# Optimization experiments

Measured on AMD Instinct MI355X. Metric: run time of the kernel, lower is better.

Reference implementation:

```python
import jax, jax.numpy as jnp
import numpy as np

B, T, D, H = 1, 4096, 1024, 16
DK = D // H
SCALE = 1.0 / float(np.sqrt(DK))
NEG = -1e9


def setup_inputs() -> dict:
    key = jax.random.key(0)
    k1, k2, k3 = jax.random.split(key, 3)
    x = jax.random.normal(k1, (B, T, D), dtype=jnp.float32)
    # xavier-ish small weights (gain 0.5)
    Wqkv = jax.random.normal(k2, (3 * D, D), dtype=jnp.float32) * 0.02
    Wout = jax.random.normal(k3, (D, D), dtype=jnp.float32) * 0.02
    return {"x": x, "Wqkv": Wqkv, "Wout": Wout}


def reference(x, Wqkv, Wout):
    b, t, d = x.shape
    # QKV projection (no bias): [B,T,3D] -> [3,B,H,T,DK]
    qkv = jnp.einsum('btd,ed->bte', x, Wqkv)
    qkv = qkv.reshape(b, t, 3, H, DK).transpose(2, 0, 3, 1, 4)
    q, k, v = qkv[0], qkv[1], qkv[2]
    # scaled dot-product scores, clamped
    scores = jnp.einsum('bhtd,bhsd->bhts', q, k) * SCALE
    scores = jnp.clip(scores, -10.0, 10.0)
    # causal additive mask (strict upper triangle gets -1e9)
    mask = jnp.triu(jnp.full((t, t), NEG, dtype=scores.dtype), k=1)
    scores = scores + mask[None, None, :, :]
    attn = jax.nn.softmax(scores, axis=-1)  # dropout is identity in eval
    out = jnp.einsum('bhts,bhsd->bhtd', attn, v)
    out = out.transpose(0, 2, 1, 3).reshape(b, t, d)
    return jnp.einsum('btd,ed->bte', out, Wout)
```

## Files before the change

kernel.cpp:

```cpp
#include <hip/hip_runtime.h>

#define T_SEQ   4096
#define D_MODEL 1024
#define NH      16
#define HD      64
#define E3      3072
#define QSCL    0.125f
#define TILEB   (64L*E3)
#define SLOTSZ  8448

using u32x2  = __attribute__((ext_vector_type(2))) unsigned int;
using u32x4  = __attribute__((ext_vector_type(4))) unsigned int;
using u16x4  = __attribute__((ext_vector_type(4))) unsigned short;
using u16x8  = __attribute__((ext_vector_type(8))) unsigned short;
using u64x2  = __attribute__((ext_vector_type(2))) unsigned long long;
using f32x4  = __attribute__((ext_vector_type(4))) float;
using bf16x8 = __attribute__((ext_vector_type(8))) __bf16;

__device__ __forceinline__ unsigned short f2bf(float f){
  unsigned int u = __builtin_bit_cast(unsigned int, f);
  u += 0x7fffu + ((u >> 16) & 1u);
  return (unsigned short)(u >> 16);
}
__device__ __forceinline__ float bf2f(unsigned short v){
  unsigned int u = ((unsigned int)v) << 16;
  return __builtin_bit_cast(float, u);
}

__device__ __forceinline__ void gload_lds16(const void* g, void* l){
  __builtin_amdgcn_global_load_lds((const __attribute__((address_space(1))) void*)g,
                                   (__attribute__((address_space(3))) void*)l, 16, 0, 0);
}

#define XN4   (T_SEQ*D_MODEL/4)
#define WQN4  (E3*D_MODEL/4)
#define WON4  (D_MODEL*D_MODEL/4)
__global__ __launch_bounds__(256) void cvt_all(const float4* __restrict__ x,
                                               const float4* __restrict__ wq,
                                               const float4* __restrict__ wo,
                                               u16x4* __restrict__ xb,
                                               u16x4* __restrict__ wqb,
                                               u16x4* __restrict__ wob){
  int i = blockIdx.x * 256 + threadIdx.x;
  const float4* src; u16x4* dst; int j;
  if(i < XN4){ src = x;  dst = xb;  j = i; }
  else if(i < XN4 + WQN4){ src = wq; dst = wqb; j = i - XN4; }
  else { src = wo; dst = wob; j = i - XN4 - WQN4; }
  float4 v = src[j];
  u16x4 o = { f2bf(v.x), f2bf(v.y), f2bf(v.z), f2bf(v.w) };
  dst[j] = o;
}

template<int OUT_BF16, int QSCALE>
__global__ __launch_bounds__(256) void gemm_bt(const unsigned short* __restrict__ A,
                                               const unsigned short* __restrict__ B,
                                               void* __restrict__ Cv,
                                               int M, int N, int K){
  __shared__ unsigned short As[128*32];
  __shared__ unsigned short Bs[128*32];
  const int t    = threadIdx.x;
  const int lane = t & 63;
  const int w    = t >> 6;
  const int brow = blockIdx.y * 128;
  const int bcol = blockIdx.x * 128;
  const int wrow = (w >> 1) * 64;
  const int wcol = (w & 1) * 64;
  const int cc = lane & 15;
  const int gg = lane >> 4;

  f32x4 acc[4][4];
  #pragma unroll
  for(int m=0;m<4;++m)
    #pragma unroll
    for(int n=0;n<4;++n)
      acc[m][n] = (f32x4){0.f,0.f,0.f,0.f};

  const int srow = t >> 2;
  const int sk   = (t & 3) * 8;
  const long aBase = (long)(brow + srow) * K;
  const long bBase = (long)(bcol + srow) * K;

  for(int k0 = 0; k0 < K; k0 += 32){
    __syncthreads();
    gload_lds16(A + aBase + k0 + sk,               As + t*8);
    gload_lds16(A + aBase + 64*(long)K + k0 + sk,  As + 2048 + t*8);
    gload_lds16(B + bBase + k0 + sk,               Bs + t*8);
    gload_lds16(B + bBase + 64*(long)K + k0 + sk,  Bs + 2048 + t*8);
    __syncthreads();

    bf16x8 af[4], bfr[4];
    #pragma unroll
    for(int m=0;m<4;++m)
      af[m]  = *(const bf16x8*)((const char*)As + (wrow + m*16 + cc)*64 + gg*16);
    #pragma unroll
    for(int n=0;n<4;++n)
      bfr[n] = *(const bf16x8*)((const char*)Bs + (wcol + n*16 + cc)*64 + gg*16);
    #pragma unroll
    for(int m=0;m<4;++m)
      #pragma unroll
      for(int n=0;n<4;++n)
        acc[m][n] = __builtin_amdgcn_mfma_f32_16x16x32_bf16(af[m], bfr[n], acc[m][n], 0, 0, 0);
  }

  #pragma unroll
  for(int m=0;m<4;++m){
    #pragma unroll
    for(int n=0;n<4;++n){
      const int row0 = brow + wrow + m*16 + gg*4;
      const int col  = bcol + wcol + n*16 + cc;
      const float sc = (QSCALE && col < D_MODEL) ? QSCL : 1.0f;
      #pragma unroll
      for(int r=0;r<4;++r){
        if constexpr (OUT_BF16 != 0){
          ((unsigned short*)Cv)[(long)(row0 + r)*N + col] = f2bf(acc[m][n][r] * sc);
        } else {
          ((float*)Cv)[(long)(row0 + r)*N + col] = acc[m][n][r];
        }
      }
    }
  }
}

__global__ __launch_bounds__(256) void gemm_bt64(const unsigned short* __restrict__ A,
                                                 const unsigned short* __restrict__ B,
                                                 float* __restrict__ C,
                                                 int M, int N, int K){
  __shared__ unsigned short As[64*32];
  __shared__ unsigned short Bs[128*32];
  const int t    = threadIdx.x;
  const int lane = t & 63;
  const int w    = t >> 6;
  const int brow = blockIdx.y * 64;
  const int bcol = blockIdx.x * 128;
  const int wrow = (w >> 1) * 32;
  const int wcol = (w & 1) * 64;
  const int cc = lane & 15;
  const int gg = lane >> 4;

  f32x4 acc[2][4];
  #pragma unroll
  for(int m=0;m<2;++m)
    #pragma unroll
    for(int n=0;n<4;++n)
      acc[m][n] = (f32x4){0.f,0.f,0.f,0.f};

  const int srow = t >> 2;
  const int sk   = (t & 3) * 8;
  const long aBase = (long)(brow + srow) * K;
  const long bBase = (long)(bcol + srow) * K;

  for(int k0 = 0; k0 < K; k0 += 32){
    __syncthreads();
    gload_lds16(A + aBase + k0 + sk,               As + t*8);
    gload_lds16(B + bBase + k0 + sk,               Bs + t*8);
    gload_lds16(B + bBase + 64*(long)K + k0 + sk,  Bs + 2048 + t*8);
    __syncthreads();

    bf16x8 af[2], bfr[4];
    #pragma unroll
    for(int m=0;m<2;++m)
      af[m]  = *(const bf16x8*)((const char*)As + (wrow + m*16 + cc)*64 + gg*16);
    #pragma unroll
    for(int n=0;n<4;++n)
      bfr[n] = *(const bf16x8*)((const char*)Bs + (wcol + n*16 + cc)*64 + gg*16);
    #pragma unroll
    for(int m=0;m<2;++m)
      #pragma unroll
      for(int n=0;n<4;++n)
        acc[m][n] = __builtin_amdgcn_mfma_f32_16x16x32_bf16(af[m], bfr[n], acc[m][n], 0, 0, 0);
  }

  #pragma unroll
  for(int m=0;m<2;++m){
    #pragma unroll
    for(int n=0;n<4;++n){
      const int row0 = brow + wrow + m*16 + gg*4;
      const int col  = bcol + wcol + n*16 + cc;
      #pragma unroll
      for(int r=0;r<4;++r)
        C[(long)(row0 + r)*N + col] = acc[m][n][r];
    }
  }
}

__global__ __launch_bounds__(256, 5) void attn_part(const unsigned short* __restrict__ qkv,
                                                    unsigned short* __restrict__ attnb,
                                                    char* __restrict__ parts){
  __shared__ char LB[32768];

  const int t    = threadIdx.x;
  const int lane = t & 63;
  const int w    = t >> 6;
  const int cc   = lane & 15;
  const int gg   = lane >> 4;

  const int bid  = blockIdx.x;
  const int hd   = bid & 15;
  const int item = 175 - (bid >> 4);

  int qb, t0, n, slot;
  if(item < 16){
    qb = item; t0 = 0; n = qb + 1; slot = -1;
  } else if(item < 48){
    const int i = item - 16; qb = 16 + (i >> 1); const int hf = i & 1;
    const int n0 = qb + 1, h0 = (n0 + 1) >> 1;
    t0 = hf ? h0 : 0; n = hf ? (n0 - h0) : h0;
    slot = (hd*16 + (qb-16))*2 + hf;
  } else {
    const int i = item - 48; qb = 32 + (i >> 2); const int qt = i & 3;
    const int n0 = qb + 1, bsz = n0 >> 2, rem = n0 & 3;
    t0 = qt*bsz + (qt < rem ? qt : rem);
    n  = bsz + (qt < rem ? 1 : 0);
    slot = 512 + (hd*32 + (qb-32))*4 + qt;
  }
  const int q0w = qb*64 + w*16;

  bf16x8 bq0 = *(const bf16x8*)(qkv + (long)(q0w+cc)*E3 + hd*HD +      gg*8);
  bf16x8 bq1 = *(const bf16x8*)(qkv + (long)(q0w+cc)*E3 + hd*HD + 32 + gg*8);

  const f32x4 z4 = (f32x4){0.f,0.f,0.f,0.f};
  const bf16x8 ones = __builtin_bit_cast(bf16x8,
      (u32x4){0x3F803F80u,0x3F803F80u,0x3F803F80u,0x3F803F80u});

  f32x4 acc0 = z4, acc1 = z4, acc2 = z4, acc3 = z4, rsacc = z4;

  const bool lb0 = (4*gg + 0) > cc;
  const bool lb1 = (4*gg + 1) > cc;
  const bool lb2 = (4*gg + 2) > cc;
  const bool lb3 = (4*gg + 3) > cc;

  const int kOffA = cc*128 + (((gg    ) ^ (cc&7)) << 4);
  const int kOffB = cc*128 + (((gg + 4) ^ (cc&7)) << 4);

  const unsigned ldsBase = (unsigned)(unsigned long long)(&LB[0]);
  const unsigned vA0 = ldsBase + 8192  + lane*8;
  const unsigned vA1 = ldsBase + 24576 + lane*8;

  const int kLane0 = (t>>3)*E3 + D_MODEL + hd*HD + (((t&7) ^ ((t>>3)&7)) << 3);
  const int kLane1 = kLane0 + 32*E3;
  const int vLane0 = (4*((t>>3)&15) + ((t&7)>>1))*E3 + 2*D_MODEL + hd*HD
                     + ((2*(t>>7) + (t&1)) << 3);
  const int vLane1 = vLane0 + 32;

  #define STAGE(g_, BUF) do{                                                       \
    const unsigned short* gb_ = qkv + (long)(g_)*TILEB;                            \
    gload_lds16(gb_ + kLane0, LB + (BUF)*16384 + t*16);                            \
    gload_lds16(gb_ + kLane1, LB + (BUF)*16384 + 4096  + t*16);                    \
    gload_lds16(gb_ + vLane0, LB + (BUF)*16384 + 8192  + t*16);                    \
    gload_lds16(gb_ + vLane1, LB + (BUF)*16384 + 12288 + t*16);                    \
  }while(0)

  #define TRRD(d_, va_, OFF_)                                                      \
    asm volatile("ds_read_b64_tr_b16 %0, %1 offset:%c2"                            \
                 : "=v"(d_) : "v"(va_), "i"(OFF_))

  #define PVH(pa_, vab_, H)                                                        \
  {                                                                                \
    unsigned long long q0_,q1_,q2_,q3_,q4_,q5_,q6_,q7_;                            \
    TRRD(q0_, vab_, (H)*1024 + 0);    TRRD(q1_, vab_, (H)*1024 + 512);             \
    TRRD(q2_, vab_, (H)*1024 + 2048); TRRD(q3_, vab_, (H)*1024 + 2560);            \
    TRRD(q4_, vab_, (H)*1024 + 4096); TRRD(q5_, vab_, (H)*1024 + 4608);            \
    TRRD(q6_, vab_, (H)*1024 + 6144); TRRD(q7_, vab_, (H)*1024 + 6656);            \
    asm volatile("s_waitcnt lgkmcnt(0)");                                          \
    __builtin_amdgcn_sched_barrier(0);                                             \
    rsacc = __builtin_amdgcn_mfma_f32_16x16x32_bf16(pa_, ones, rsacc, 0,0,0);      \
    u64x2 p0_ = {q0_,q1_};                                                         \
    acc0 = __builtin_amdgcn_mfma_f32_16x16x32_bf16(pa_, __builtin_bit_cast(bf16x8,p0_), acc0, 0,0,0); \
    u64x2 p1_ = {q2_,q3_};                                                         \
    acc1 = __builtin_amdgcn_mfma_f32_16x16x32_bf16(pa_, __builtin_bit_cast(bf16x8,p1_), acc1, 0,0,0); \
    u64x2 p2_ = {q4_,q5_};                                                         \
    acc2 = __builtin_amdgcn_mfma_f32_16x16x32_bf16(pa_, __builtin_bit_cast(bf16x8,p2_), acc2, 0,0,0); \
    u64x2 p3_ = {q6_,q7_};                                                         \
    acc3 = __builtin_amdgcn_mfma_f32_16x16x32_bf16(pa_, __builtin_bit_cast(bf16x8,p3_), acc3, 0,0,0); \
  }

  #define TILE(g_, BUF)                                                            \
  {                                                                                \
    STAGE((g_)+1, (BUF)^1);                                                        \
    float pk[4][4];                                                                \
    const bool last_ = ((g_) == qb);                                               \
    if(!last_){                                                                    \
      _Pragma("unroll")                                                            \
      for(int kt=0; kt<4; ++kt){                                                   \
        bf16x8 a0 = *(const bf16x8*)(LB + (BUF)*16384 + kOffA + kt*2048);          \
        bf16x8 a1 = *(const bf16x8*)(LB + (BUF)*16384 + kOffB + kt*2048);          \
        f32x4 s = __builtin_amdgcn_mfma_f32_16x16x32_bf16(a0, bq0, z4, 0,0,0);     \
        s = __builtin_amdgcn_mfma_f32_16x16x32_bf16(a1, bq1, s, 0,0,0);            \
        pk[kt][0] = __expf(__builtin_amdgcn_fmed3f(s[0],-10.f,10.f));              \
        pk[kt][1] = __expf(__builtin_amdgcn_fmed3f(s[1],-10.f,10.f));              \
        pk[kt][2] = __expf(__builtin_amdgcn_fmed3f(s[2],-10.f,10.f));              \
        pk[kt][3] = __expf(__builtin_amdgcn_fmed3f(s[3],-10.f,10.f));              \
      }                                                                            \
    } else {                                                                       \
      _Pragma("unroll")                                                            \
      for(int kt=0; kt<4; ++kt){                                                   \
        if(kt <= w){                                                               \
          bf16x8 a0 = *(const bf16x8*)(LB + (BUF)*16384 + kOffA + kt*2048);        \
          bf16x8 a1 = *(const bf16x8*)(LB + (BUF)*16384 + kOffB + kt*2048);        \
          f32x4 s = __builtin_amdgcn_mfma_f32_16x16x32_bf16(a0, bq0, z4, 0,0,0);   \
          s = __builtin_amdgcn_mfma_f32_16x16x32_bf16(a1, bq1, s, 0,0,0);          \
          float p0_ = __expf(__builtin_amdgcn_fmed3f(s[0],-10.f,10.f));            \
          float p1_ = __expf(__builtin_amdgcn_fmed3f(s[1],-10.f,10.f));            \
          float p2_ = __expf(__builtin_amdgcn_fmed3f(s[2],-10.f,10.f));            \
          float p3_ = __expf(__builtin_amdgcn_fmed3f(s[3],-10.f,10.f));            \
          if(kt == w){                                                             \
            p0_ = lb0 ? 0.f : p0_;  p1_ = lb1 ? 0.f : p1_;                         \
            p2_ = lb2 ? 0.f : p2_;  p3_ = lb3 ? 0.f : p3_;                         \
          }                                                                        \
          pk[kt][0]=p0_; pk[kt][1]=p1_; pk[kt][2]=p2_; pk[kt][3]=p3_;              \
        } else {                                                                   \
          pk[kt][0]=0.f; pk[kt][1]=0.f; pk[kt][2]=0.f; pk[kt][3]=0.f;              \
        }                                                                          \
      }                                                                            \
    }                                                                              \
    bf16x8 pa0 = (bf16x8){ (__bf16)pk[0][0],(__bf16)pk[0][1],(__bf16)pk[0][2],     \
      (__bf16)pk[0][3],(__bf16)pk[1][0],(__bf16)pk[1][1],(__bf16)pk[1][2],         \
      (__bf16)pk[1][3] };                                                          \
    bf16x8 pa1 = (bf16x8){ (__bf16)pk[2][0],(__bf16)pk[2][1],(__bf16)pk[2][2],     \
      (__bf16)pk[2][3],(__bf16)pk[3][0],(__bf16)pk[3][1],(__bf16)pk[3][2],         \
      (__bf16)pk[3][3] };                                                          \
    const unsigned vab_ = (BUF) ? vA1 : vA0;                                       \
    PVH(pa0, vab_, 0);                                                             \
    if(!last_ || w >= 2){ PVH(pa1, vab_, 1); }                                     \
    __syncthreads();                                                               \
  }

  STAGE(t0, 0);
  __syncthreads();

  int lt = 0;
  while(lt + 2 <= n){
    TILE(t0+lt,   0);
    TILE(t0+lt+1, 1);
    lt += 2;
  }
  if(lt < n) TILE(t0+lt, 0);

  if(slot < 0){
    #pragma unroll
    for(int rr=0;rr<4;++rr){
      const float inv = 1.0f / rsacc[rr];
      const int row = q0w + 4*gg + rr;
      unsigned short* dst = attnb + (long)row*D_MODEL + hd*HD + cc;
      dst[0]  = __builtin_bit_cast(unsigned short, (__bf16)(acc0[rr]*inv));
      dst[16] = __builtin_bit_cast(unsigned short, (__bf16)(acc1[rr]*inv));
      dst[32] = __builtin_bit_cast(unsigned short, (__bf16)(acc2[rr]*inv));
      dst[48] = __builtin_bit_cast(unsigned short, (__bf16)(acc3[rr]*inv));
    }
  } else {
    char* sp = parts + (size_t)slot * SLOTSZ;
    #pragma unroll
    for(int rr=0;rr<4;++rr){
      const int row = w*16 + 4*gg + rr;
      unsigned short* dst = (unsigned short*)sp + row*64 + cc;
      dst[0]  = f2bf(acc0[rr]);
      dst[16] = f2bf(acc1[rr]);
      dst[32] = f2bf(acc2[rr]);
      dst[48] = f2bf(acc3[rr]);
      if(cc == 0) ((float*)(sp + 8192))[row] = rsacc[rr];
    }
  }
  #undef STAGE
  #undef TRRD
  #undef PVH
  #undef TILE
}

__global__ __launch_bounds__(256) void attn_combine(const char* __restrict__ parts,
                                                    unsigned short* __restrict__ attnb){
  const int b  = blockIdx.x;
  const int hd = b & 15;
  const int qb = 16 + (b >> 4);
  const int t  = threadIdx.x;
  const int r  = t >> 2;
  const int d0 = (t & 3) * 16;

  const char* p0; int np;
  if(qb < 32){ p0 = parts + (size_t)((hd*16 + (qb-16))*2) * SLOTSZ;        np = 2; }
  else       { p0 = parts + (size_t)(512 + (hd*32 + (qb-32))*4) * SLOTSZ;  np = 4; }

  float rs = 0.f;
  float o[16];
  #pragma unroll
  for(int j=0;j<16;++j) o[j] = 0.f;

  for(int pi = 0; pi < np; ++pi){
    const char* pp = p0 + (size_t)pi * SLOTSZ;
    rs += ((const float*)(pp + 8192))[r];
    u16x8 a0 = *(const u16x8*)(pp + (r*64 + d0)*2);
    u16x8 a1 = *(const u16x8*)(pp + (r*64 + d0)*2 + 16);
    #pragma unroll
    for(int j=0;j<8;++j){ o[j] += bf2f(a0[j]); o[8+j] += bf2f(a1[j]); }
  }
  const float inv = 1.0f / rs;
  u16x8 o0, o1;
  #pragma unroll
  for(int j=0;j<8;++j){ o0[j] = f2bf(o[j]*inv); o1[j] = f2bf(o[8+j]*inv); }
  unsigned short* dst = attnb + (long)(qb*64 + r)*D_MODEL + hd*HD + d0;
  *(u16x8*)(dst)     = o0;
  *(u16x8*)(dst + 8) = o1;
}

extern "C" void kernel_launch(void* const* d_in, const int* in_sizes, int n_in,
                              void* d_out, int out_size, void* d_ws, size_t ws_size,
                              hipStream_t stream){
  (void)in_sizes; (void)n_in; (void)out_size; (void)ws_size;
  const float* x    = (const float*)d_in[0];
  const float* wqkv = (const float*)d_in[1];
  const float* wout = (const float*)d_in[2];
  char* ws = (char*)d_ws;
  unsigned short* woutb = (unsigned short*)(ws);
  unsigned short* attnb = (unsigned short*)(ws + (2u  << 20));
  unsigned short* qkvb  = (unsigned short*)(ws + (10u << 20));
  unsigned short* xb    = (unsigned short*)(ws + (34u << 20));
  unsigned short* wqkvb = (unsigned short*)(ws + (42u << 20));
  char*           parts = ws + (34u << 20);
  float* out = (float*)d_out;

  cvt_all<<<dim3((XN4 + WQN4 + WON4)/256), 256, 0, stream>>>(
      (const float4*)x, (const float4*)wqkv, (const float4*)wout,
      (u16x4*)xb, (u16x4*)wqkvb, (u16x4*)woutb);

  dim3 g1(E3/128, T_SEQ/128);
  gemm_bt<1,1><<<g1, 256, 0, stream>>>(xb, wqkvb, qkvb, T_SEQ, E3, D_MODEL);

  attn_part<<<dim3(176*NH), 256, 0, stream>>>(qkvb, attnb, parts);
  attn_combine<<<dim3(48*NH), 256, 0, stream>>>(parts, attnb);

  dim3 g3(D_MODEL/128, T_SEQ/64);
  gemm_bt64<<<g3, 256, 0, stream>>>(attnb, woutb, out, T_SEQ, D_MODEL, D_MODEL);
}
```

Measured before the change: 127.9 us.

## Software-pipeline attention loop: overlap next tile QK/softmax with current PV

Restructures the attention inner loop so the QK^T scores and softmax for tile i+1 are computed while the PV MFMAs for tile i are issued, interleaving LDS reads and matrix ops. K and V staging are split into separate double-buffered LDS regions, with K prefetched two tiles ahead and V one tile ahead. The aim is to hide exp/softmax latency and LDS read latency behind MFMA work. It costs extra registers for the carried probability fragments and uses more complex buffer indexing, which may lower occupancy.

```diff
diff --git a/kernel.cpp b/kernel.cpp
--- a/kernel.cpp
+++ b/kernel.cpp
@@ -224,16 +224,11 @@
 
   f32x4 acc0 = z4, acc1 = z4, acc2 = z4, acc3 = z4, rsacc = z4;
 
-  const bool lb0 = (4*gg + 0) > cc;
-  const bool lb1 = (4*gg + 1) > cc;
-  const bool lb2 = (4*gg + 2) > cc;
-  const bool lb3 = (4*gg + 3) > cc;
-
   const int kOffA = cc*128 + (((gg    ) ^ (cc&7)) << 4);
   const int kOffB = cc*128 + (((gg + 4) ^ (cc&7)) << 4);
 
   const unsigned ldsBase = (unsigned)(unsigned long long)(&LB[0]);
-  const unsigned vA0 = ldsBase + 8192  + lane*8;
+  const unsigned vA0 = ldsBase + 16384 + lane*8;
   const unsigned vA1 = ldsBase + 24576 + lane*8;
 
   const int kLane0 = (t>>3)*E3 + D_MODEL + hd*HD + (((t&7) ^ ((t>>3)&7)) << 3);
@@ -242,12 +237,16 @@
                      + ((2*(t>>7) + (t&1)) << 3);
   const int vLane1 = vLane0 + 32;
 
-  #define STAGE(g_, BUF) do{                                                       \
+  #define STAGE_K(g_, B) do{                                                       \
     const unsigned short* gb_ = qkv + (long)(g_)*TILEB;                            \
-    gload_lds16(gb_ + kLane0, LB + (BUF)*16384 + t*16);                            \
-    gload_lds16(gb_ + kLane1, LB + (BUF)*16384 + 4096  + t*16);                    \
-    gload_lds16(gb_ + vLane0, LB + (BUF)*16384 + 8192  + t*16);                    \
-    gload_lds16(gb_ + vLane1, LB + (BUF)*16384 + 12288 + t*16);                    \
+    gload_lds16(gb_ + kLane0, LB + (B)*8192 + t*16);                               \
+    gload_lds16(gb_ + kLane1, LB + (B)*8192 + 4096 + t*16);                        \
+  }while(0)
+
+  #define STAGE_V(g_, B) do{                                                       \
+    const unsigned short* gb_ = qkv + (long)(g_)*TILEB;                            \
+    gload_lds16(gb_ + vLane0, LB + 16384 + (B)*8192 + t*16);                       \
+    gload_lds16(gb_ + vLane1, LB + 16384 + (B)*8192 + 4096 + t*16);                \
   }while(0)
 
   #define TRRD(d_, va_, OFF_)                                                      \
@@ -274,67 +273,88 @@
     acc3 = __builtin_amdgcn_mfma_f32_16x16x32_bf16(pa_, __builtin_bit_cast(bf16x8,p3_), acc3, 0,0,0); \
   }
 
-  #define TILE(g_, BUF)                                                            \
-  {                                                                                \
-    STAGE((g_)+1, (BUF)^1);                                                        \
-    float pk[4][4];                                                                \
-    const bool last_ = ((g_) == qb);                                               \
-    if(!last_){                                                                    \
+  #define QKRD2(kb_, KT, aa0_, aa1_) do{                                           \
+    aa0_ = *(const bf16x8*)((kb_) + kOffA + (KT)*2048);                            \
+    aa1_ = *(const bf16x8*)((kb_) + kOffB + (KT)*2048);                            \
+  }while(0)
+
+  #define QKMM(aa0_, aa1_, sd_) do{                                               \
+    sd_ = __builtin_amdgcn_mfma_f32_16x16x32_bf16(aa0_, bq0, z4, 0,0,0);           \
+    sd_ = __builtin_amdgcn_mfma_f32_16x16x32_bf16(aa1_, bq1, sd_, 0,0,0);          \
+  }while(0)
+
+  #define SMX(dl_, paO0, paO1) do{                                                 \
+    f32x4 sv_[4] = {s0, s1, s2, s3};                                               \
+    float pkv[4][4];                                                               \
+    _Pragma("unroll")                                                              \
+    for(int kt=0; kt<4; ++kt){                                                     \
       _Pragma("unroll")                                                            \
-      for(int kt=0; kt<4; ++kt){                                                   \
-        bf16x8 a0 = *(const bf16x8*)(LB + (BUF)*16384 + kOffA + kt*2048);          \
-        bf16x8 a1 = *(const bf16x8*)(LB + (BUF)*16384 + kOffB + kt*2048);          \
-        f32x4 s = __builtin_amdgcn_mfma_f32_16x16x32_bf16(a0, bq0, z4, 0,0,0);     \
-        s = __builtin_amdgcn_mfma_f32_16x16x32_bf16(a1, bq1, s, 0,0,0);            \
-        pk[kt][0] = __expf(__builtin_amdgcn_fmed3f(s[0],-10.f,10.f));              \
-        pk[kt][1] = __expf(__builtin_amdgcn_fmed3f(s[1],-10.f,10.f));              \
-        pk[kt][2] = __expf(__builtin_amdgcn_fmed3f(s[2],-10.f,10.f));              \
-        pk[kt][3] = __expf(__builtin_amdgcn_fmed3f(s[3],-10.f,10.f));              \
-      }                                                                            \
-    } else {                                                                       \
-      _Pragma("unroll")                                                            \
-      for(int kt=0; kt<4; ++kt){                                                   \
-        if(kt <= w){                                                               \
-          bf16x8 a0 = *(const bf16x8*)(LB + (BUF)*16384 + kOffA + kt*2048);        \
-          bf16x8 a1 = *(const bf16x8*)(LB + (BUF)*16384 + kOffB + kt*2048);        \
-          f32x4 s = __builtin_amdgcn_mfma_f32_16x16x32_bf16(a0, bq0, z4, 0,0,0);   \
-          s = __builtin_amdgcn_mfma_f32_16x16x32_bf16(a1, bq1, s, 0,0,0);          \
-          float p0_ = __expf(__builtin_amdgcn_fmed3f(s[0],-10.f,10.f));            \
-          float p1_ = __expf(__builtin_amdgcn_fmed3f(s[1],-10.f,10.f));            \
-          float p2_ = __expf(__builtin_amdgcn_fmed3f(s[2],-10.f,10.f));            \
-          float p3_ = __expf(__builtin_amdgcn_fmed3f(s[3],-10.f,10.f));            \
-          if(kt == w){                                                             \
-            p0_ = lb0 ? 0.f : p0_;  p1_ = lb1 ? 0.f : p1_;                         \
-            p2_ = lb2 ? 0.f : p2_;  p3_ = lb3 ? 0.f : p3_;                         \
-          }                                                                        \
-          pk[kt][0]=p0_; pk[kt][1]=p1_; pk[kt][2]=p2_; pk[kt][3]=p3_;              \
-        } else {                                                                   \
-          pk[kt][0]=0.f; pk[kt][1]=0.f; pk[kt][2]=0.f; pk[kt][3]=0.f;              \
+      for(int rr=0; rr<4; ++rr){                                                   \
+        float p_ = __expf(__builtin_amdgcn_fmed3f(sv_[kt][rr], -10.f, 10.f));      \
+        if(dl_){                                                                   \
+          if(kt > w) p_ = 0.f;                                                     \
+          else if(kt == w && ((4*gg + rr) > cc)) p_ = 0.f;                         \
         }                                                                          \
+        pkv[kt][rr] = p_;                                                          \
       }                                                                            \
     }                                                                              \
-    bf16x8 pa0 = (bf16x8){ (__bf16)pk[0][0],(__bf16)pk[0][1],(__bf16)pk[0][2],     \
-      (__bf16)pk[0][3],(__bf16)pk[1][0],(__bf16)pk[1][1],(__bf16)pk[1][2],         \
-      (__bf16)pk[1][3] };                                                          \
-    bf16x8 pa1 = (bf16x8){ (__bf16)pk[2][0],(__bf16)pk[2][1],(__bf16)pk[2][2],     \
-      (__bf16)pk[2][3],(__bf16)pk[3][0],(__bf16)pk[3][1],(__bf16)pk[3][2],         \
-      (__bf16)pk[3][3] };                                                          \
-    const unsigned vab_ = (BUF) ? vA1 : vA0;                                       \
-    PVH(pa0, vab_, 0);                                                             \
-    if(!last_ || w >= 2){ PVH(pa1, vab_, 1); }                                     \
+    paO0 = (bf16x8){ (__bf16)pkv[0][0],(__bf16)pkv[0][1],(__bf16)pkv[0][2],(__bf16)pkv[0][3], \
+                     (__bf16)pkv[1][0],(__bf16)pkv[1][1],(__bf16)pkv[1][2],(__bf16)pkv[1][3] };\
+    paO1 = (bf16x8){ (__bf16)pkv[2][0],(__bf16)pkv[2][1],(__bf16)pkv[2][2],(__bf16)pkv[2][3], \
+                     (__bf16)pkv[3][0],(__bf16)pkv[3][1],(__bf16)pkv[3][2],(__bf16)pkv[3][3] };\
+  }while(0)
+
+  #define ITER(i_, KQB, VB, paI0, paI1, paO0, paO1)                                \
+  {                                                                                \
+    const int g_ = t0 + (i_);                                                      \
+    const bool haveN_ = ((i_) + 1 < n);                                            \
+    const bool doH1_ = (g_ != qb) || (w >= 2);                                     \
+    if((i_) + 2 < n) STAGE_K(g_+2, (KQB)^1);                                       \
+    if(haveN_)       STAGE_V(g_+1, (VB)^1);                                        \
+    const unsigned vb_ = (VB) ? vA1 : vA0;                                         \
+    if(haveN_){                                                                    \
+      const char* kb_ = (const char*)LB + (KQB)*8192;                              \
+      const bool dl_ = ((g_ + 1) == qb);                                           \
+      bf16x8 a00,a01,a10,a11; f32x4 s0,s1,s2,s3;                                   \
+      QKRD2(kb_, 0, a00, a01); QKRD2(kb_, 1, a10, a11);                            \
+      PVH(paI0, vb_, 0);                                                           \
+      QKMM(a00, a01, s0); QKMM(a10, a11, s1);                                      \
+      QKRD2(kb_, 2, a00, a01); QKRD2(kb_, 3, a10, a11);                            \
+      if(doH1_){ PVH(paI1, vb_, 1); }                                              \
+      QKMM(a00, a01, s2); QKMM(a10, a11, s3);                                      \
+      SMX(dl_, paO0, paO1);                                                        \
+    } else {                                                                       \
+      PVH(paI0, vb_, 0);                                                           \
+      if(doH1_){ PVH(paI1, vb_, 1); }                                              \
+    }                                                                              \
     __syncthreads();                                                               \
   }
 
-  STAGE(t0, 0);
+  STAGE_K(t0, 0);
+  STAGE_V(t0, 0);
+  STAGE_K(t0+1, 1);
   __syncthreads();
 
-  int lt = 0;
-  while(lt + 2 <= n){
-    TILE(t0+lt,   0);
-    TILE(t0+lt+1, 1);
-    lt += 2;
-  }
-  if(lt < n) TILE(t0+lt, 0);
+  bf16x8 paA0, paA1, paB0, paB1;
+  {
+    const bool dl_ = (t0 == qb);
+    bf16x8 a00,a01,a10,a11; f32x4 s0,s1,s2,s3;
+    const char* kb_ = (const char*)LB;
+    QKRD2(kb_, 0, a00, a01); QKRD2(kb_, 1, a10, a11);
+    QKMM(a00, a01, s0); QKMM(a10, a11, s1);
+    QKRD2(kb_, 2, a00, a01); QKRD2(kb_, 3, a10, a11);
+    QKMM(a00, a01, s2); QKMM(a10, a11, s3);
+    SMX(dl_, paA0, paA1);
+    paB0 = paA0; paB1 = paA1;
+  }
+
+  int i = 0;
+  while(i + 2 <= n){
+    ITER(i,   1, 0, paA0, paA1, paB0, paB1);
+    ITER(i+1, 0, 1, paB0, paB1, paA0, paA1);
+    i += 2;
+  }
+  if(i < n) ITER(i, 1, 0, paA0, paA1, paB0, paB1);
 
   if(slot < 0){
     #pragma unroll
@@ -360,10 +380,14 @@
       if(cc == 0) ((float*)(sp + 8192))[row] = rsacc[rr];
     }
   }
-  #undef STAGE
+  #undef STAGE_K
+  #undef STAGE_V
   #undef TRRD
   #undef PVH
-  #undef TILE
+  #undef QKRD2
+  #undef QKMM
+  #undef SMX
+  #undef ITER
 }
 
 __global__ __launch_bounds__(256) void attn_combine(const char* __restrict__ parts,
```

New measurement: 183.7 us. +43.6%, slower.

## Process two query blocks per attention workgroup to reuse staged K/V tiles

Applied to the files above, without the earlier changes.

Each attention workgroup now handles 128 query rows (two 64-row blocks) against each staged K/V tile, halving K/V global-to-LDS traffic per query row and the grid size. Row sums move from an extra MFMA against a ones vector to scalar accumulation followed by cross-lane shuffles. Partial results use larger slots, with overflow placed in the output buffer as scratch before the final GEMM overwrites it. More registers per thread lower occupancy to 4 waves per SIMD, and fewer, larger work items may balance worse across CUs.

```diff
diff --git a/kernel.cpp b/kernel.cpp
--- a/kernel.cpp
+++ b/kernel.cpp
@@ -7,7 +7,8 @@
 #define E3      3072
 #define QSCL    0.125f
 #define TILEB   (64L*E3)
-#define SLOTSZ  8448
+#define SLOTSZ  16896
+#define P0CAP   800
 
 using u32x2  = __attribute__((ext_vector_type(2))) unsigned int;
 using u32x4  = __attribute__((ext_vector_type(4))) unsigned int;
@@ -30,6 +31,11 @@
 __device__ __forceinline__ void gload_lds16(const void* g, void* l){
   __builtin_amdgcn_global_load_lds((const __attribute__((address_space(1))) void*)g,
                                    (__attribute__((address_space(3))) void*)l, 16, 0, 0);
+}
+
+__device__ __forceinline__ char* part_ptr(char* p0, char* p1, int slot){
+  return (slot < P0CAP) ? p0 + (size_t)slot * SLOTSZ
+                        : p1 + (size_t)(slot - P0CAP) * SLOTSZ;
 }
 
 #define XN4   (T_SEQ*D_MODEL/4)
@@ -183,9 +189,10 @@
   }
 }
 
-__global__ __launch_bounds__(256, 5) void attn_part(const unsigned short* __restrict__ qkv,
+__global__ __launch_bounds__(256, 4) void attn_part(const unsigned short* __restrict__ qkv,
                                                     unsigned short* __restrict__ attnb,
-                                                    char* __restrict__ parts){
+                                                    char* __restrict__ parts0,
+                                                    char* __restrict__ parts1){
   __shared__ char LB[32768];
 
   const int t    = threadIdx.x;
@@ -196,38 +203,37 @@
 
   const int bid  = blockIdx.x;
   const int hd   = bid & 15;
-  const int item = 175 - (bid >> 4);
-
-  int qb, t0, n, slot;
-  if(item < 16){
-    qb = item; t0 = 0; n = qb + 1; slot = -1;
-  } else if(item < 48){
-    const int i = item - 16; qb = 16 + (i >> 1); const int hf = i & 1;
-    const int n0 = qb + 1, h0 = (n0 + 1) >> 1;
-    t0 = hf ? h0 : 0; n = hf ? (n0 - h0) : h0;
-    slot = (hd*16 + (qb-16))*2 + hf;
+  const int o_   = bid >> 4;
+  const int item = (o_ < 8) ? (7 - o_) : (95 - o_);
+
+  int QB, t0, n, slot;
+  if(item < 8){
+    QB = item; t0 = 0; n = 2*QB + 2; slot = -1;
+  } else if(item < 24){
+    const int i = item - 8; QB = 8 + (i >> 1); const int hf = i & 1;
+    const int h0 = QB + 1;
+    t0 = hf * h0; n = h0;
+    slot = (hd*8 + (QB-8))*2 + hf;
   } else {
-    const int i = item - 48; qb = 32 + (i >> 2); const int qt = i & 3;
-    const int n0 = qb + 1, bsz = n0 >> 2, rem = n0 & 3;
+    const int i = item - 24; QB = 16 + (i >> 2); const int qt = i & 3;
+    const int n0 = 2*QB + 2, bsz = n0 >> 2, rem = n0 & 3;
     t0 = qt*bsz + (qt < rem ? qt : rem);
     n  = bsz + (qt < rem ? 1 : 0);
-    slot = 512 + (hd*32 + (qb-32))*4 + qt;
-  }
-  const int q0w = qb*64 + w*16;
-
-  bf16x8 bq0 = *(const bf16x8*)(qkv + (long)(q0w+cc)*E3 + hd*HD +      gg*8);
-  bf16x8 bq1 = *(const bf16x8*)(qkv + (long)(q0w+cc)*E3 + hd*HD + 32 + gg*8);
+    slot = 256 + (hd*16 + (QB-16))*4 + qt;
+  }
+  const int gA = 2*QB;
+  const int gB = 2*QB + 1;
+  const int qA = QB*128 + w*16;
+
+  bf16x8 bqA0 = *(const bf16x8*)(qkv + (long)(qA+cc)*E3 + hd*HD +      gg*8);
+  bf16x8 bqA1 = *(const bf16x8*)(qkv + (long)(qA+cc)*E3 + hd*HD + 32 + gg*8);
+  bf16x8 bqB0 = *(const bf16x8*)(qkv + (long)(qA+64+cc)*E3 + hd*HD +      gg*8);
+  bf16x8 bqB1 = *(const bf16x8*)(qkv + (long)(qA+64+cc)*E3 + hd*HD + 32 + gg*8);
 
   const f32x4 z4 = (f32x4){0.f,0.f,0.f,0.f};
-  const bf16x8 ones = __builtin_bit_cast(bf16x8,
-      (u32x4){0x3F803F80u,0x3F803F80u,0x3F803F80u,0x3F803F80u});
-
-  f32x4 acc0 = z4, acc1 = z4, acc2 = z4, acc3 = z4, rsacc = z4;
-
-  const bool lb0 = (4*gg + 0) > cc;
-  const bool lb1 = (4*gg + 1) > cc;
-  const bool lb2 = (4*gg + 2) > cc;
-  const bool lb3 = (4*gg + 3) > cc;
+  f32x4 accA0=z4, accA1=z4, accA2=z4, accA3=z4;
+  f32x4 accB0=z4, accB1=z4, accB2=z4, accB3=z4;
+  float rsA = 0.f, rsB = 0.f;
 
   const int kOffA = cc*128 + (((gg    ) ^ (cc&7)) << 4);
   const int kOffB = cc*128 + (((gg + 4) ^ (cc&7)) << 4);
@@ -254,7 +260,12 @@
     asm volatile("ds_read_b64_tr_b16 %0, %1 offset:%c2"                            \
                  : "=v"(d_) : "v"(va_), "i"(OFF_))
 
-  #define PVH(pa_, vab_, H)                                                        \
+  #define PACKA(KT, RR, P) do{ if((KT)<2) paA0[(KT)*4+(RR)] = (__bf16)(P);         \
+                               else        paA1[((KT)-2)*4+(RR)] = (__bf16)(P); }while(0)
+  #define PACKB(KT, RR, P) do{ if((KT)<2) paB0[(KT)*4+(RR)] = (__bf16)(P);         \
+                               else        paB1[((KT)-2)*4+(RR)] = (__bf16)(P); }while(0)
+
+  #define PVHALF(vab_, H, DOA, DOB)                                                \
   {                                                                                \
     unsigned long long q0_,q1_,q2_,q3_,q4_,q5_,q6_,q7_;                            \
     TRRD(q0_, vab_, (H)*1024 + 0);    TRRD(q1_, vab_, (H)*1024 + 512);             \
@@ -263,65 +274,103 @@
     TRRD(q6_, vab_, (H)*1024 + 6144); TRRD(q7_, vab_, (H)*1024 + 6656);            \
     asm volatile("s_waitcnt lgkmcnt(0)");                                          \
     __builtin_amdgcn_sched_barrier(0);                                             \
-    rsacc = __builtin_amdgcn_mfma_f32_16x16x32_bf16(pa_, ones, rsacc, 0,0,0);      \
-    u64x2 p0_ = {q0_,q1_};                                                         \
-    acc0 = __builtin_amdgcn_mfma_f32_16x16x32_bf16(pa_, __builtin_bit_cast(bf16x8,p0_), acc0, 0,0,0); \
-    u64x2 p1_ = {q2_,q3_};                                                         \
-    acc1 = __builtin_amdgcn_mfma_f32_16x16x32_bf16(pa_, __builtin_bit_cast(bf16x8,p1_), acc1, 0,0,0); \
-    u64x2 p2_ = {q4_,q5_};                                                         \
-    acc2 = __builtin_amdgcn_mfma_f32_16x16x32_bf16(pa_, __builtin_bit_cast(bf16x8,p2_), acc2, 0,0,0); \
-    u64x2 p3_ = {q6_,q7_};                                                         \
-    acc3 = __builtin_amdgcn_mfma_f32_16x16x32_bf16(pa_, __builtin_bit_cast(bf16x8,p3_), acc3, 0,0,0); \
+    u64x2 w0_ = {q0_,q1_}; bf16x8 bv0_ = __builtin_bit_cast(bf16x8, w0_);          \
+    u64x2 w1_ = {q2_,q3_}; bf16x8 bv1_ = __builtin_bit_cast(bf16x8, w1_);          \
+    u64x2 w2_ = {q4_,q5_}; bf16x8 bv2_ = __builtin_bit_cast(bf16x8, w2_);          \
+    u64x2 w3_ = {q6_,q7_}; bf16x8 bv3_ = __builtin_bit_cast(bf16x8, w3_);          \
+    if(DOA){                                                                       \
+      bf16x8 pa_ = (H) ? paA1 : paA0;                                              \
+      accA0 = __builtin_amdgcn_mfma_f32_16x16x32_bf16(pa_, bv0_, accA0, 0,0,0);    \
+      accA1 = __builtin_amdgcn_mfma_f32_16x16x32_bf16(pa_, bv1_, accA1, 0,0,0);    \
+      accA2 = __builtin_amdgcn_mfma_f32_16x16x32_bf16(pa_, bv2_, accA2, 0,0,0);    \
+      accA3 = __builtin_amdgcn_mfma_f32_16x16x32_bf16(pa_, bv3_, accA3, 0,0,0);    \
+    }                                                                              \
+    if(DOB){                                                                       \
+      bf16x8 pb_ = (H) ? paB1 : paB0;                                              \
+      accB0 = __builtin_amdgcn_mfma_f32_16x16x32_bf16(pb_, bv0_, accB0, 0,0,0);    \
+      accB1 = __builtin_amdgcn_mfma_f32_16x16x32_bf16(pb_, bv1_, accB1, 0,0,0);    \
+      accB2 = __builtin_amdgcn_mfma_f32_16x16x32_bf16(pb_, bv2_, accB2, 0,0,0);    \
+      accB3 = __builtin_amdgcn_mfma_f32_16x16x32_bf16(pb_, bv3_, accB3, 0,0,0);    \
+    }                                                                              \
   }
 
   #define TILE(g_, BUF)                                                            \
   {                                                                                \
     STAGE((g_)+1, (BUF)^1);                                                        \
-    float pk[4][4];                                                                \
-    const bool last_ = ((g_) == qb);                                               \
-    if(!last_){                                                                    \
+    bf16x8 paA0, paA1, paB0, paB1;                                                 \
+    const char* kb_ = (const char*)LB + (BUF)*16384;                               \
+    if((g_) < gA){                                                                 \
       _Pragma("unroll")                                                            \
       for(int kt=0; kt<4; ++kt){                                                   \
-        bf16x8 a0 = *(const bf16x8*)(LB + (BUF)*16384 + kOffA + kt*2048);          \
-        bf16x8 a1 = *(const bf16x8*)(LB + (BUF)*16384 + kOffB + kt*2048);          \
-        f32x4 s = __builtin_amdgcn_mfma_f32_16x16x32_bf16(a0, bq0, z4, 0,0,0);     \
-        s = __builtin_amdgcn_mfma_f32_16x16x32_bf16(a1, bq1, s, 0,0,0);            \
-        pk[kt][0] = __expf(__builtin_amdgcn_fmed3f(s[0],-10.f,10.f));              \
-        pk[kt][1] = __expf(__builtin_amdgcn_fmed3f(s[1],-10.f,10.f));              \
-        pk[kt][2] = __expf(__builtin_amdgcn_fmed3f(s[2],-10.f,10.f));              \
-        pk[kt][3] = __expf(__builtin_amdgcn_fmed3f(s[3],-10.f,10.f));              \
+        bf16x8 a0 = *(const bf16x8*)(kb_ + kOffA + kt*2048);                       \
+        bf16x8 a1 = *(const bf16x8*)(kb_ + kOffB + kt*2048);                       \
+        f32x4 sA = __builtin_amdgcn_mfma_f32_16x16x32_bf16(a0, bqA0, z4, 0,0,0);   \
+        sA = __builtin_amdgcn_mfma_f32_16x16x32_bf16(a1, bqA1, sA, 0,0,0);         \
+        f32x4 sB = __builtin_amdgcn_mfma_f32_16x16x32_bf16(a0, bqB0, z4, 0,0,0);   \
+        sB = __builtin_amdgcn_mfma_f32_16x16x32_bf16(a1, bqB1, sB, 0,0,0);         \
+        _Pragma("unroll")                                                          \
+        for(int rr=0; rr<4; ++rr){                                                 \
+          float pA_ = __expf(__builtin_amdgcn_fmed3f(sA[rr], -10.f, 10.f));        \
+          float pB_ = __expf(__builtin_amdgcn_fmed3f(sB[rr], -10.f, 10.f));        \
+          rsA += pA_; rsB += pB_;                                                  \
+          PACKA(kt, rr, pA_); PACKB(kt, rr, pB_);                                  \
+        }                                                                          \
       }                                                                            \
     } else {                                                                       \
+      const bool dA_ = ((g_) == gA);                   \
+      paA0 = paA1 = __builtin_bit_cast(bf16x8, (u32x4){0u,0u,0u,0u});              \
       _Pragma("unroll")                                                            \
       for(int kt=0; kt<4; ++kt){                                                   \
-        if(kt <= w){                                                               \
-          bf16x8 a0 = *(const bf16x8*)(LB + (BUF)*16384 + kOffA + kt*2048);        \
-          bf16x8 a1 = *(const bf16x8*)(LB + (BUF)*16384 + kOffB + kt*2048);        \
-          f32x4 s = __builtin_amdgcn_mfma_f32_16x16x32_bf16(a0, bq0, z4, 0,0,0);   \
-          s = __builtin_amdgcn_mfma_f32_16x16x32_bf16(a1, bq1, s, 0,0,0);          \
-          float p0_ = __expf(__builtin_amdgcn_fmed3f(s[0],-10.f,10.f));            \
-          float p1_ = __expf(__builtin_amdgcn_fmed3f(s[1],-10.f,10.f));            \
-          float p2_ = __expf(__builtin_amdgcn_fmed3f(s[2],-10.f,10.f));            \
-          float p3_ = __expf(__builtin_amdgcn_fmed3f(s[3],-10.f,10.f));            \
-          if(kt == w){                                                             \
-            p0_ = lb0 ? 0.f : p0_;  p1_ = lb1 ? 0.f : p1_;                         \
-            p2_ = lb2 ? 0.f : p2_;  p3_ = lb3 ? 0.f : p3_;                         \
+        bf16x8 a0 = *(const bf16x8*)(kb_ + kOffA + kt*2048);                       \
+        bf16x8 a1 = *(const bf16x8*)(kb_ + kOffB + kt*2048);                       \
+        if(dA_){                                                                   \
+                                               \
+          f32x4 sB = __builtin_amdgcn_mfma_f32_16x16x32_bf16(a0, bqB0, z4, 0,0,0); \
+          sB = __builtin_amdgcn_mfma_f32_16x16x32_bf16(a1, bqB1, sB, 0,0,0);       \
+          if(kt <= w){                                                             \
+            f32x4 sA = __builtin_amdgcn_mfma_f32_16x16x32_bf16(a0, bqA0, z4, 0,0,0);\
+            sA = __builtin_amdgcn_mfma_f32_16x16x32_bf16(a1, bqA1, sA, 0,0,0);     \
+            _Pragma("unroll")                                                      \
+            for(int rr=0; rr<4; ++rr){                                             \
+              float pA_ = __expf(__builtin_amdgcn_fmed3f(sA[rr], -10.f, 10.f));    \
+              if(kt == w && ((4*gg + rr) > cc)) pA_ = 0.f;                         \
+              rsA += pA_; PACKA(kt, rr, pA_);                                      \
+            }                                                                      \
           }                                                                        \
-          pk[kt][0]=p0_; pk[kt][1]=p1_; pk[kt][2]=p2_; pk[kt][3]=p3_;              \
+          _Pragma("unroll")                                                        \
+          for(int rr=0; rr<4; ++rr){                                               \
+            float pB_ = __expf(__builtin_amdgcn_fmed3f(sB[rr], -10.f, 10.f));      \
+            rsB += pB_; PACKB(kt, rr, pB_);                                        \
+          }                                                                        \
         } else {                                                                   \
-          pk[kt][0]=0.f; pk[kt][1]=0.f; pk[kt][2]=0.f; pk[kt][3]=0.f;              \
+                                     \
+          if(kt <= w){                                                             \
+            f32x4 sB = __builtin_amdgcn_mfma_f32_16x16x32_bf16(a0, bqB0, z4, 0,0,0);\
+            sB = __builtin_amdgcn_mfma_f32_16x16x32_bf16(a1, bqB1, sB, 0,0,0);     \
+            _Pragma("unroll")                                                      \
+            for(int rr=0; rr<4; ++rr){                                             \
+              float pB_ = __expf(__builtin_amdgcn_fmed3f(sB[rr], -10.f, 10.f));    \
+              if(kt == w && ((4*gg + rr) > cc)) pB_ = 0.f;                         \
+              rsB += pB_; PACKB(kt, rr, pB_);                                      \
+            }                                                                      \
+          } else {                                                                 \
+            _Pragma("unroll")                                                      \
+            for(int rr=0; rr<4; ++rr) PACKB(kt, rr, 0.f);                          \
+          }                                                                        \
         }                                                                          \
       }                                                                            \
     }                                                                              \
-    bf16x8 pa0 = (bf16x8){ (__bf16)pk[0][0],(__bf16)pk[0][1],(__bf16)pk[0][2],     \
-      (__bf16)pk[0][3],(__bf16)pk[1][0],(__bf16)pk[1][1],(__bf16)pk[1][2],         \
-      (__bf16)pk[1][3] };                                                          \
-    bf16x8 pa1 = (bf16x8){ (__bf16)pk[2][0],(__bf16)pk[2][1],(__bf16)pk[2][2],     \
-      (__bf16)pk[2][3],(__bf16)pk[3][0],(__bf16)pk[3][1],(__bf16)pk[3][2],         \
-      (__bf16)pk[3][3] };                                                          \
     const unsigned vab_ = (BUF) ? vA1 : vA0;                                       \
-    PVH(pa0, vab_, 0);                                                             \
-    if(!last_ || w >= 2){ PVH(pa1, vab_, 1); }                                     \
+    if((g_) < gA){                                                                 \
+      PVHALF(vab_, 0, 1, 1);                                                       \
+      PVHALF(vab_, 1, 1, 1);                                                       \
+    } else if((g_) == gA){                                                         \
+      PVHALF(vab_, 0, 1, 1);                                                       \
+      if(w >= 2){ PVHALF(vab_, 1, 1, 1); } else { PVHALF(vab_, 1, 0, 1); }         \
+    } else {                                                                       \
+      PVHALF(vab_, 0, 0, 1);                                                       \
+      if(w >= 2){ PVHALF(vab_, 1, 0, 1); }                                         \
+    }                                                                              \
     __syncthreads();                                                               \
   }
 
@@ -336,69 +385,93 @@
   }
   if(lt < n) TILE(t0+lt, 0);
 
+  rsA += __shfl_xor(rsA, 16);  rsA += __shfl_xor(rsA, 32);
+  rsB += __shfl_xor(rsB, 16);  rsB += __shfl_xor(rsB, 32);
+
   if(slot < 0){
     #pragma unroll
     for(int rr=0;rr<4;++rr){
-      const float inv = 1.0f / rsacc[rr];
-      const int row = q0w + 4*gg + rr;
-      unsigned short* dst = attnb + (long)row*D_MODEL + hd*HD + cc;
-      dst[0]  = __builtin_bit_cast(unsigned short, (__bf16)(acc0[rr]*inv));
-      dst[16] = __builtin_bit_cast(unsigned short, (__bf16)(acc1[rr]*inv));
-      dst[32] = __builtin_bit_cast(unsigned short, (__bf16)(acc2[rr]*inv));
-      dst[48] = __builtin_bit_cast(unsigned short, (__bf16)(acc3[rr]*inv));
+      const float invA = 1.0f / __shfl(rsA, 4*gg + rr);
+      const int rowA = qA + 4*gg + rr;
+      unsigned short* dA = attnb + (long)rowA*D_MODEL + hd*HD + cc;
+      dA[0]  = __builtin_bit_cast(unsigned short, (__bf16)(accA0[rr]*invA));
+      dA[16] = __builtin_bit_cast(unsigned short, (__bf16)(accA1[rr]*invA));
+      dA[32] = __builtin_bit_cast(unsigned short, (__bf16)(accA2[rr]*invA));
+      dA[48] = __builtin_bit_cast(unsigned short, (__bf16)(accA3[rr]*invA));
+      const float invB = 1.0f / __shfl(rsB, 4*gg + rr);
+      unsigned short* dB = dA + 64L*D_MODEL;
+      dB[0]  = __builtin_bit_cast(unsigned short, (__bf16)(accB0[rr]*invB));
+      dB[16] = __builtin_bit_cast(unsigned short, (__bf16)(accB1[rr]*invB));
+      dB[32] = __builtin_bit_cast(unsigned short, (__bf16)(accB2[rr]*invB));
+      dB[48] = __builtin_bit_cast(unsigned short, (__bf16)(accB3[rr]*invB));
     }
   } else {
-    char* sp = parts + (size_t)slot * SLOTSZ;
+    char* sp = part_ptr(parts0, parts1, slot);
     #pragma unroll
     for(int rr=0;rr<4;++rr){
-      const int row = w*16 + 4*gg + rr;
-      unsigned short* dst = (unsigned short*)sp + row*64 + cc;
-      dst[0]  = f2bf(acc0[rr]);
-      dst[16] = f2bf(acc1[rr]);
-      dst[32] = f2bf(acc2[rr]);
-      dst[48] = f2bf(acc3[rr]);
-      if(cc == 0) ((float*)(sp + 8192))[row] = rsacc[rr];
+      const int rowA = w*16 + 4*gg + rr;
+      unsigned short* dA = (unsigned short*)sp + rowA*64 + cc;
+      dA[0]  = f2bf(accA0[rr]);
+      dA[16] = f2bf(accA1[rr]);
+      dA[32] = f2bf(accA2[rr]);
+      dA[48] = f2bf(accA3[rr]);
+      unsigned short* dB = dA + 64*64;
+      dB[0]  = f2bf(accB0[rr]);
+      dB[16] = f2bf(accB1[rr]);
+      dB[32] = f2bf(accB2[rr]);
+      dB[48] = f2bf(accB3[rr]);
+    }
+    if(gg == 0){
+      ((float*)(sp + 16384))[w*16 + cc]      = rsA;
+      ((float*)(sp + 16384))[64 + w*16 + cc] = rsB;
     }
   }
   #undef STAGE
   #undef TRRD
-  #undef PVH
+  #undef PACKA
+  #undef PACKB
+  #undef PVHALF
   #undef TILE
 }
 
-__global__ __launch_bounds__(256) void attn_combine(const char* __restrict__ parts,
+__global__ __launch_bounds__(256) void attn_combine(char* __restrict__ parts0,
+                                                    char* __restrict__ parts1,
                                                     unsigned short* __restrict__ attnb){
   const int b  = blockIdx.x;
   const int hd = b & 15;
-  const int qb = 16 + (b >> 4);
+  const int QB = 8 + (b >> 4);
   const int t  = threadIdx.x;
-  const int r  = t >> 2;
-  const int d0 = (t & 3) * 16;
-
-  const char* p0; int np;
-  if(qb < 32){ p0 = parts + (size_t)((hd*16 + (qb-16))*2) * SLOTSZ;        np = 2; }
-  else       { p0 = parts + (size_t)(512 + (hd*32 + (qb-32))*4) * SLOTSZ;  np = 4; }
+  const int r  = t >> 1;
+  const int d0 = (t & 1) * 32;
+
+  int s0_, np;
+  if(QB < 16){ s0_ = (hd*8 + (QB-8))*2;        np = 2; }
+  else       { s0_ = 256 + (hd*16 + (QB-16))*4; np = 4; }
 
   float rs = 0.f;
-  float o[16];
+  float o[32];
   #pragma unroll
-  for(int j=0;j<16;++j) o[j] = 0.f;
+  for(int j=0;j<32;++j) o[j] = 0.f;
 
   for(int pi = 0; pi < np; ++pi){
-    const char* pp = p0 + (size_t)pi * SLOTSZ;
-    rs += ((const float*)(pp + 8192))[r];
-    u16x8 a0 = *(const u16x8*)(pp + (r*64 + d0)*2);
-    u16x8 a1 = *(const u16x8*)(pp + (r*64 + d0)*2 + 16);
-    #pragma unroll
-    for(int j=0;j<8;++j){ o[j] += bf2f(a0[j]); o[8+j] += bf2f(a1[j]); }
+    const char* pp = part_ptr(parts0, parts1, s0_ + pi);
+    rs += ((const float*)(pp + 16384))[r];
+    #pragma unroll
+    for(int q=0;q<4;++q){
+      u16x8 a = *(const u16x8*)(pp + (r*64 + d0 + q*8)*2);
+      #pragma unroll
+      for(int j=0;j<8;++j) o[q*8+j] += bf2f(a[j]);
+    }
   }
   const float inv = 1.0f / rs;
-  u16x8 o0, o1;
+  unsigned short* dst = attnb + (long)(QB*128 + r)*D_MODEL + hd*HD + d0;
   #pragma unroll
-  for(int j=0;j<8;++j){ o0[j] = f2bf(o[j]*inv); o1[j] = f2bf(o[8+j]*inv); }
-  unsigned short* dst = attnb + (long)(qb*64 + r)*D_MODEL + hd*HD + d0;
-  *(u16x8*)(dst)     = o0;
-  *(u16x8*)(dst + 8) = o1;
+  for(int q=0;q<4;++q){
+    u16x8 ov;
+    #pragma unroll
+    for(int j=0;j<8;++j) ov[j] = f2bf(o[q*8+j]*inv);
+    *(u16x8*)(dst + q*8) = ov;
+  }
 }
 
 extern "C" void kernel_launch(void* const* d_in, const int* in_sizes, int n_in,
@@ -414,7 +487,8 @@
   unsigned short* qkvb  = (unsigned short*)(ws + (10u << 20));
   unsigned short* xb    = (unsigned short*)(ws + (34u << 20));
   unsigned short* wqkvb = (unsigned short*)(ws + (42u << 20));
-  char*           parts = ws + (34u << 20);
+  char*           parts0 = ws + (34u << 20);
+  char*           parts1 = (char*)d_out;
   float* out = (float*)d_out;
 
   cvt_all<<<dim3((XN4 + WQN4 + WON4)/256), 256, 0, stream>>>(
@@ -424,8 +498,8 @@
   dim3 g1(E3/128, T_SEQ/128);
   gemm_bt<1,1><<<g1, 256, 0, stream>>>(xb, wqkvb, qkvb, T_SEQ, E3, D_MODEL);
 
-  attn_part<<<dim3(176*NH), 256, 0, stream>>>(qkvb, attnb, parts);
-  attn_combine<<<dim3(48*NH), 256, 0, stream>>>(parts, attnb);
+  attn_part<<<dim3(88*NH), 256, 0, stream>>>(qkvb, attnb, parts0, parts1);
+  attn_combine<<<dim3(24*NH), 256, 0, stream>>>(parts0, parts1, attnb);
 
   dim3 g3(D_MODEL/128, T_SEQ/64);
   gemm_bt64<<<g3, 256, 0, stream>>>(attnb, woutb, out, T_SEQ, D_MODEL, D_MODEL);
```

New measurement: 144.7 us. +13.1%, slower.
